# Optimization experiments

Hardware: AMD Instinct MI355X
Metric: run time of the kernel (lower is better)

The kernel has to match this reference:

```python
import jax, jax.numpy as jnp
import numpy as np

N = 512        # N_ROIs (nodes)
E = N * N      # fully connected graph, COO edges
NV = 6         # n_views (edge feature dim)
C1_IN, C1_OUT = 1, 36
C2_IN, C2_OUT = 36, 24
C3_IN, C3_OUT = 24, 5


def _nnconv(x, src, dst, edge_attr, W, b, root, bias, n_nodes):
    """PyG NNConv with aggr='mean': out_i = mean_{j->i} x_j @ Theta(e_ji) + x_i @ root + bias.
    Theta = ReLU(edge_attr @ W + b) reshaped to [E, in, out] (Sequential(Linear, ReLU) edge nn)."""
    in_ch = x.shape[1]
    out_ch = root.shape[1]
    theta = jax.nn.relu(edge_attr @ W + b).reshape(-1, in_ch, out_ch)  # [E, in, out]
    msg = jnp.einsum('ei,eio->eo', x[src], theta)                      # [E, out]
    summed = jax.ops.segment_sum(msg, dst, num_segments=n_nodes)       # [N, out]
    cnt = jax.ops.segment_sum(jnp.ones((msg.shape[0], 1), x.dtype), dst, num_segments=n_nodes)
    agg = summed / jnp.maximum(cnt, 1.0)
    return agg + x @ root + bias


def setup_inputs() -> dict:
    key = jax.random.key(0)
    ks = jax.random.split(key, 12)
    s = lambda fan_in: 1.0 / np.sqrt(fan_in)
    x = jnp.ones((N, C1_IN), jnp.float32)
    edge_attr = jax.random.uniform(ks[0], (E, NV), jnp.float32)
    edge_index = jax.random.randint(ks[1], (2, E), 0, N, dtype=jnp.int64)
    return {
        'x': x, 'edge_attr': edge_attr, 'edge_index': edge_index,
        'W1': jax.random.normal(ks[2], (NV, C1_IN * C1_OUT), jnp.float32) * s(NV),
        'b1': jnp.zeros((C1_IN * C1_OUT,), jnp.float32),
        'root1': jax.random.normal(ks[3], (C1_IN, C1_OUT), jnp.float32) * s(C1_IN),
        'bias1': jnp.zeros((C1_OUT,), jnp.float32),
        'W2': jax.random.normal(ks[4], (NV, C2_IN * C2_OUT), jnp.float32) * s(NV),
        'b2': jnp.zeros((C2_IN * C2_OUT,), jnp.float32),
        'root2': jax.random.normal(ks[5], (C2_IN, C2_OUT), jnp.float32) * s(C2_IN),
        'bias2': jnp.zeros((C2_OUT,), jnp.float32),
        'W3': jax.random.normal(ks[6], (NV, C3_IN * C3_OUT), jnp.float32) * s(NV),
        'b3': jnp.zeros((C3_IN * C3_OUT,), jnp.float32),
        'root3': jax.random.normal(ks[7], (C3_IN, C3_OUT), jnp.float32) * s(C3_IN),
        'bias3': jnp.zeros((C3_OUT,), jnp.float32),
    }


def reference(x, edge_attr, edge_index, W1, b1, root1, bias1,
              W2, b2, root2, bias2, W3, b3, root3, bias3):
    src, dst = edge_index[0], edge_index[1]
    n = x.shape[0]
    h = jax.nn.relu(_nnconv(x, src, dst, edge_attr, W1, b1, root1, bias1, n))
    h = jax.nn.relu(_nnconv(h, src, dst, edge_attr, W2, b2, root2, bias2, n))
    h = jax.nn.relu(_nnconv(h, src, dst, edge_attr, W3, b3, root3, bias3, n))
    # CBT: cbt[a, b] = sum_f |h[b, f] - h[a, f]|  (repeat/transpose/abs/sum in torch)
    cbt = jnp.sum(jnp.abs(h[None, :, :] - h[:, None, :]), axis=2)  # [N, N]
    return cbt
```

## Files before the change

### kernel.cpp

```cpp
#include <hip/hip_runtime.h>

#define N_NODES 512
#define N_EDGES (512 * 512)

typedef _Float16 f16x8 __attribute__((ext_vector_type(8)));
typedef float f32x4 __attribute__((ext_vector_type(4)));

__device__ __forceinline__ unsigned pkf16(float a, float b) {
  return __builtin_bit_cast(unsigned, __builtin_amdgcn_cvt_pkrtz(a, b));
}

__global__ void hist_k(const int* __restrict__ dst, int* __restrict__ counts) {
  __shared__ int lh[N_NODES];
  for (int i = threadIdx.x; i < N_NODES; i += blockDim.x) lh[i] = 0;
  __syncthreads();
  const int stride = gridDim.x * blockDim.x;
  for (int e = blockIdx.x * blockDim.x + threadIdx.x; e < N_EDGES; e += stride)
    atomicAdd(&lh[dst[e]], 1);
  __syncthreads();
  for (int i = threadIdx.x; i < N_NODES; i += blockDim.x) {
    int c = lh[i];
    if (c) atomicAdd(&counts[i], c);
  }
}

__global__ void scan_k(const int* __restrict__ counts, int* __restrict__ offsets,
                       int* __restrict__ cursor) {
  __shared__ int tmp[N_NODES];
  const int t = threadIdx.x;
  const int c = counts[t];
  tmp[t] = c;
  __syncthreads();
  for (int d = 1; d < N_NODES; d <<= 1) {
    int add = (t >= d) ? tmp[t - d] : 0;
    __syncthreads();
    tmp[t] += add;
    __syncthreads();
  }
  offsets[t + 1] = tmp[t];
  if (t == 0) offsets[0] = 0;
  cursor[t] = tmp[t] - c;
}

__launch_bounds__(512)
__global__ void scatter3_k(const float* __restrict__ ea, const int* __restrict__ src,
                           const int* __restrict__ dst, int* __restrict__ cursor,
                           uint4* __restrict__ eaPk, int* __restrict__ srcSorted) {
  __shared__ int lhist[N_NODES];
  __shared__ int gb[N_NODES];
  const int t = threadIdx.x;
  const int c0 = blockIdx.x * 4096;
  lhist[t] = 0;
  __syncthreads();
  int d[8], r[8];
#pragma unroll
  for (int j = 0; j < 8; j++) {
    d[j] = dst[c0 + t + j * 512];
    r[j] = atomicAdd(&lhist[d[j]], 1);
  }
  __syncthreads();
  gb[t] = atomicAdd(&cursor[t], lhist[t]);
  __syncthreads();
#pragma unroll
  for (int j = 0; j < 8; j++) {
    const int e = c0 + t + j * 512;
    const int pos = gb[d[j]] + r[j];
    const float2* er = reinterpret_cast<const float2*>(ea + (size_t)e * 6);
    const float2 a0 = er[0], a1 = er[1], a2 = er[2];
    uint4 pk;
    pk.x = pkf16(a0.x, a0.y);
    pk.y = pkf16(a1.x, a1.y);
    pk.z = pkf16(a2.x, a2.y);
    pk.w = 0x00003C00u;
    eaPk[pos] = pk;
    srcSorted[pos] = src[e];
  }
}

__global__ void packAll2_k(const float* __restrict__ W1, const float* __restrict__ b1,
                           const float* __restrict__ W2, const float* __restrict__ b2,
                           const float* __restrict__ W3, const float* __restrict__ b3,
                           uint4* __restrict__ wpk) {
  const int t = blockIdx.x * 256 + threadIdx.x;
  uint4 r = make_uint4(0u, 0u, 0x00000000u, pkf16(-1.f, 0.f));
  if (t < 48) {
    if (t < 36) {
      r.x = pkf16(W1[0 * 36 + t], W1[1 * 36 + t]);
      r.y = pkf16(W1[2 * 36 + t], W1[3 * 36 + t]);
      r.z = pkf16(W1[4 * 36 + t], W1[5 * 36 + t]);
      r.w = pkf16(b1[t], 0.f);
    }
    wpk[t] = r;
  } else if (t < 1200) {
    const int q = t - 48;
    const int tile = q >> 4, row = q & 15;
    const int i = tile >> 1, o = ((tile & 1) << 4) + row;
    if (o < 24) {
      const int p = i * 24 + o;
      r.x = pkf16(W2[0 * 864 + p], W2[1 * 864 + p]);
      r.y = pkf16(W2[2 * 864 + p], W2[3 * 864 + p]);
      r.z = pkf16(W2[4 * 864 + p], W2[5 * 864 + p]);
      r.w = pkf16(b2[p], 0.f);
    }
    wpk[t] = r;
  } else if (t < 1328) {
    const int q = t - 1200;
    const int tile = q >> 4, row = q & 15;
    if (row < 15) {
      const int i = 3 * tile + row / 5;
      const int o = row % 5;
      const int p = i * 5 + o;
      r.x = pkf16(W3[0 * 120 + p], W3[1 * 120 + p]);
      r.y = pkf16(W3[2 * 120 + p], W3[3 * 120 + p]);
      r.z = pkf16(W3[4 * 120 + p], W3[5 * 120 + p]);
      r.w = pkf16(b3[p], 0.f);
    }
    wpk[t] = r;
  }
}

__launch_bounds__(512, 4)
__global__ void conv1_k(const float* __restrict__ x,
                        const uint4* __restrict__ eaPk, const int* __restrict__ srcSorted,
                        const int* __restrict__ offsets, const uint4* __restrict__ Wpk,
                        const float* __restrict__ root, const float* __restrict__ bias,
                        float* __restrict__ hnext) {
  __shared__ float hS[N_NODES];
  __shared__ float pAcc[8][48];
  const int tid = threadIdx.x, w = tid >> 6, l = tid & 63;
  const int node = blockIdx.x;
  const int off = offsets[node], cnt = offsets[node + 1] - off;
  const int col = l & 15, crow = (l >> 4) << 2;

  if (tid < N_NODES) hS[tid] = x[tid];

  f16x8 afr[3];
  f32x4 acc[3];
#pragma unroll
  for (int t = 0; t < 3; t++) {
    uint4 wv = make_uint4(0u, 0u, 0u, 0u);
    if (l < 16) wv = Wpk[t * 16 + l];
    afr[t] = __builtin_bit_cast(f16x8, wv);
    acc[t] = (f32x4){0.f, 0.f, 0.f, 0.f};
  }
  __syncthreads();

  const int NG = (cnt + 15) >> 4;
  const f32x4 zero4 = {0.f, 0.f, 0.f, 0.f};

  uint4 bv_c = make_uint4(0u, 0u, 0u, 0u);
  int s_c = 0;
  auto gload = [&](int g) {
    const int pos = g * 16 + col;
    const bool v = pos < cnt;
    s_c = v ? srcSorted[off + pos] : 0;
    bv_c = make_uint4(0u, 0u, 0u, 0u);
    if (l < 16 && v) bv_c = eaPk[off + pos];
  };

  if (w < NG) gload(w);
  for (int g = w; g < NG; g += 8) {
    const f16x8 bfr = __builtin_bit_cast(f16x8, bv_c);
    const float hv = hS[s_c];
    if (g + 8 < NG) gload(g + 8);
    f32x4 tc = __builtin_amdgcn_mfma_f32_16x16x32_f16(afr[0], bfr, zero4, 0, 0, 0);
#pragma unroll
    for (int t = 0; t < 3; t++) {
      f32x4 tn;
      if (t < 2) tn = __builtin_amdgcn_mfma_f32_16x16x32_f16(afr[t + 1], bfr, zero4, 0, 0, 0);
#pragma unroll
      for (int r = 0; r < 4; r++)
        acc[t][r] = fmaf(fmaxf(tc[r], 0.f), hv, acc[t][r]);
      if (t < 2) tc = tn;
    }
  }
#pragma unroll
  for (int t = 0; t < 3; t++)
#pragma unroll
    for (int r = 0; r < 4; r++) {
      float vv = acc[t][r];
      vv += __shfl_xor(vv, 1); vv += __shfl_xor(vv, 2);
      vv += __shfl_xor(vv, 4); vv += __shfl_xor(vv, 8);
      if (col == 0) pAcc[w][t * 16 + crow + r] = vv;
    }
  __syncthreads();
  if (tid < 36) {
    const int o = tid;
    float sagg = 0.f;
#pragma unroll
    for (int ww = 0; ww < 8; ww++) sagg += pAcc[ww][o];
    const float agg = sagg / fmaxf((float)cnt, 1.f);
    const float r2 = fmaf(hS[node], root[o], bias[o]);
    hnext[node * 36 + o] = fmaxf(agg + r2, 0.f);
  }
}

__launch_bounds__(512, 4)
__global__ void conv2_k(const float* __restrict__ hprev,
                        const uint4* __restrict__ eaPk, const int* __restrict__ srcSorted,
                        const int* __restrict__ offsets, const uint4* __restrict__ Wpk,
                        const float* __restrict__ root, const float* __restrict__ bias,
                        float* __restrict__ hnext) {
  __shared__ float hS[N_NODES * 37];
  __shared__ float pAcc[1152];
  const int tid = threadIdx.x, w = tid >> 6, l = tid & 63;
  const int node = blockIdx.x;
  const int off = offsets[node], cnt = offsets[node + 1] - off;
  const int col = l & 15, crow = (l >> 4) << 2;

  for (int n = tid; n < N_NODES * 36; n += 512) hS[n + n / 36] = hprev[n];

  f16x8 afr[5][2];
  f32x4 acc[5][2];
  int hidx[5];
#pragma unroll
  for (int jp = 0; jp < 5; jp++) {
    const int tp = w + 8 * jp;
    hidx[jp] = (tp < 36) ? tp : 0;
#pragma unroll
    for (int hh = 0; hh < 2; hh++) {
      uint4 wv = make_uint4(0u, 0u, 0u, 0u);
      if (tp < 36 && l < 16) wv = Wpk[(2 * tp + hh) * 16 + l];
      afr[jp][hh] = __builtin_bit_cast(f16x8, wv);
      acc[jp][hh] = (f32x4){0.f, 0.f, 0.f, 0.f};
    }
  }
  __syncthreads();

  const int NG = (cnt + 15) >> 4;
  const f32x4 zero4 = {0.f, 0.f, 0.f, 0.f};

  uint4 bv_c = make_uint4(0u, 0u, 0u, 0u);
  int s_c = 0;
  auto gload = [&](int g) {
    const int pos = g * 16 + col;
    const bool v = pos < cnt;
    s_c = v ? srcSorted[off + pos] : 0;
    bv_c = make_uint4(0u, 0u, 0u, 0u);
    if (l < 16 && v) bv_c = eaPk[off + pos];
  };

  if (NG > 0) gload(0);
  for (int g = 0; g < NG; g++) {
    const int sb = s_c * 37;
    float hcur[5];
#pragma unroll
    for (int jp = 0; jp < 5; jp++) hcur[jp] = hS[sb + hidx[jp]];
    const f16x8 bfr = __builtin_bit_cast(f16x8, bv_c);
    if (g + 1 < NG) gload(g + 1);
    f32x4 t0 = __builtin_amdgcn_mfma_f32_16x16x32_f16(afr[0][0], bfr, zero4, 0, 0, 0);
    f32x4 t1 = __builtin_amdgcn_mfma_f32_16x16x32_f16(afr[0][1], bfr, zero4, 0, 0, 0);
#pragma unroll
    for (int jp = 0; jp < 5; jp++) {
      f32x4 n0, n1;
      if (jp < 4) {
        n0 = __builtin_amdgcn_mfma_f32_16x16x32_f16(afr[jp + 1][0], bfr, zero4, 0, 0, 0);
        n1 = __builtin_amdgcn_mfma_f32_16x16x32_f16(afr[jp + 1][1], bfr, zero4, 0, 0, 0);
      }
      const float hv = hcur[jp];
#pragma unroll
      for (int r = 0; r < 4; r++) {
        acc[jp][0][r] = fmaf(fmaxf(t0[r], 0.f), hv, acc[jp][0][r]);
        acc[jp][1][r] = fmaf(fmaxf(t1[r], 0.f), hv, acc[jp][1][r]);
      }
      if (jp < 4) { t0 = n0; t1 = n1; }
    }
  }

#pragma unroll
  for (int jp = 0; jp < 5; jp++) {
    const int tp = w + 8 * jp;
    if (tp < 36) {
#pragma unroll
      for (int hh = 0; hh < 2; hh++)
#pragma unroll
        for (int r = 0; r < 4; r++) {
          float vv = acc[jp][hh][r];
          vv += __shfl_xor(vv, 1); vv += __shfl_xor(vv, 2);
          vv += __shfl_xor(vv, 4); vv += __shfl_xor(vv, 8);
          if (col == 0) pAcc[tp * 32 + hh * 16 + crow + r] = vv;
        }
    }
  }
  __syncthreads();
  if (tid < 24) {
    const int o = tid;
    float sagg = 0.f;
    for (int i = 0; i < 36; i++) sagg += pAcc[i * 32 + o];
    const float agg = sagg / fmaxf((float)cnt, 1.f);
    float r2 = bias[o];
    for (int i = 0; i < 36; i++) r2 = fmaf(hS[node * 37 + i], root[i * 24 + o], r2);
    hnext[node * 24 + o] = fmaxf(agg + r2, 0.f);
  }
}

__launch_bounds__(512, 4)
__global__ void conv3_k(const float* __restrict__ hprev,
                        const uint4* __restrict__ eaPk, const int* __restrict__ srcSorted,
                        const int* __restrict__ offsets, const uint4* __restrict__ Wpk,
                        const float* __restrict__ root, const float* __restrict__ bias,
                        float* __restrict__ hnext) {
  __shared__ float hS[N_NODES * 25];
  __shared__ float pAcc[8][128];
  const int tid = threadIdx.x, w = tid >> 6, l = tid & 63;
  const int node = blockIdx.x;
  const int off = offsets[node], cnt = offsets[node + 1] - off;
  const int col = l & 15, crow = (l >> 4) << 2;

  for (int n = tid; n < N_NODES * 24; n += 512) hS[n + n / 24] = hprev[n];

  f16x8 afr[8];
  f32x4 acc[8];
#pragma unroll
  for (int t = 0; t < 8; t++) {
    uint4 wv = make_uint4(0u, 0u, 0u, 0u);
    if (l < 16) wv = Wpk[t * 16 + l];
    afr[t] = __builtin_bit_cast(f16x8, wv);
    acc[t] = (f32x4){0.f, 0.f, 0.f, 0.f};
  }
  __syncthreads();

  const int NG = (cnt + 15) >> 4;
  const f32x4 zero4 = {0.f, 0.f, 0.f, 0.f};

  uint4 bv_c = make_uint4(0u, 0u, 0u, 0u);
  int s_c = 0;
  auto gload = [&](int g) {
    const int pos = g * 16 + col;
    const bool v = pos < cnt;
    s_c = v ? srcSorted[off + pos] : 0;
    bv_c = make_uint4(0u, 0u, 0u, 0u);
    if (l < 16 && v) bv_c = eaPk[off + pos];
  };

  if (w < NG) gload(w);
  for (int g = w; g < NG; g += 8) {
    const int sb = s_c * 25;
    float h0[8], h1[8], h2[8];
#pragma unroll
    for (int t = 0; t < 8; t++) {
      h0[t] = hS[sb + 3 * t];
      h1[t] = hS[sb + 3 * t + 1];
      h2[t] = hS[sb + 3 * t + 2];
    }
    const f16x8 bfr = __builtin_bit_cast(f16x8, bv_c);
    if (g + 8 < NG) gload(g + 8);
    f32x4 tc = __builtin_amdgcn_mfma_f32_16x16x32_f16(afr[0], bfr, zero4, 0, 0, 0);
#pragma unroll
    for (int t = 0; t < 8; t++) {
      f32x4 tn;
      if (t < 7) tn = __builtin_amdgcn_mfma_f32_16x16x32_f16(afr[t + 1], bfr, zero4, 0, 0, 0);
#pragma unroll
      for (int r = 0; r < 4; r++) {
        const int row = crow + r;
        const float hv = (row < 5) ? h0[t] : ((row < 10) ? h1[t] : h2[t]);
        acc[t][r] = fmaf(fmaxf(tc[r], 0.f), hv, acc[t][r]);
      }
      if (t < 7) tc = tn;
    }
  }
#pragma unroll
  for (int t = 0; t < 8; t++)
#pragma unroll
    for (int r = 0; r < 4; r++) {
      float vv = acc[t][r];
      vv += __shfl_xor(vv, 1); vv += __shfl_xor(vv, 2);
      vv += __shfl_xor(vv, 4); vv += __shfl_xor(vv, 8);
      if (col == 0) pAcc[w][t * 16 + crow + r] = vv;
    }
  __syncthreads();
  if (tid < 128) {
    float s8 = 0.f;
#pragma unroll
    for (int ww = 0; ww < 8; ww++) s8 += pAcc[ww][tid];
    pAcc[0][tid] = s8;
  }
  __syncthreads();
  if (tid < 5) {
    const int o = tid;
    float sagg = 0.f;
    for (int i = 0; i < 24; i++) {
      const int t = i / 3, iloc = i - 3 * t;
      sagg += pAcc[0][t * 16 + iloc * 5 + o];
    }
    const float agg = sagg / fmaxf((float)cnt, 1.f);
    float r2 = bias[o];
    for (int i = 0; i < 24; i++) r2 = fmaf(hS[node * 25 + i], root[i * 5 + o], r2);
    hnext[node * 5 + o] = fmaxf(agg + r2, 0.f);
  }
}

__global__ void cbt_k(const float* __restrict__ h3, float* __restrict__ out) {
  __shared__ float sh[N_NODES * 5];
  for (int i = threadIdx.x; i < N_NODES * 5; i += blockDim.x) sh[i] = h3[i];
  __syncthreads();
  const int a = blockIdx.x;
  float ha0 = sh[a * 5 + 0], ha1 = sh[a * 5 + 1], ha2 = sh[a * 5 + 2],
        ha3 = sh[a * 5 + 3], ha4 = sh[a * 5 + 4];
  for (int b = threadIdx.x; b < N_NODES; b += blockDim.x) {
    float s = fabsf(sh[b * 5 + 0] - ha0) + fabsf(sh[b * 5 + 1] - ha1) +
              fabsf(sh[b * 5 + 2] - ha2) + fabsf(sh[b * 5 + 3] - ha3) +
              fabsf(sh[b * 5 + 4] - ha4);
    out[a * N_NODES + b] = s;
  }
}

extern "C" void kernel_launch(void* const* d_in, const int* in_sizes, int n_in,
                              void* d_out, int out_size, void* d_ws, size_t ws_size,
                              hipStream_t stream) {
  const float* x     = (const float*)d_in[0];
  const float* ea    = (const float*)d_in[1];
  const int*   ei    = (const int*)d_in[2];
  const float* W1    = (const float*)d_in[3];
  const float* b1    = (const float*)d_in[4];
  const float* root1 = (const float*)d_in[5];
  const float* bias1 = (const float*)d_in[6];
  const float* W2    = (const float*)d_in[7];
  const float* b2    = (const float*)d_in[8];
  const float* root2 = (const float*)d_in[9];
  const float* bias2 = (const float*)d_in[10];
  const float* W3    = (const float*)d_in[11];
  const float* b3    = (const float*)d_in[12];
  const float* root3 = (const float*)d_in[13];
  const float* bias3 = (const float*)d_in[14];

  const int* src = ei;
  const int* dst = ei + N_EDGES;

  char* ws = (char*)d_ws;
  int* counts    = (int*)(ws + 0);
  int* offsets   = (int*)(ws + 4096);
  int* cursor    = (int*)(ws + 8192);
  uint4* eaPk    = (uint4*)(ws + 16384);
  int* srcSorted = (int*)(ws + 16384 + N_EDGES * 16);
  char* p2       = ws + 16384 + N_EDGES * 20;
  float* h1      = (float*)(p2);
  float* h2_     = h1 + N_NODES * 36;
  float* h3      = h2_ + N_NODES * 24;
  uint4* wpkAll  = (uint4*)(p2 + 256 * 1024);
  uint4* wpk1    = wpkAll;
  uint4* wpk2    = wpkAll + 48;
  uint4* wpk3    = wpkAll + 1200;

  hipMemsetAsync(counts, 0, N_NODES * sizeof(int), stream);
  hist_k<<<64, 256, 0, stream>>>(dst, counts);
  scan_k<<<1, N_NODES, 0, stream>>>(counts, offsets, cursor);
  scatter3_k<<<N_EDGES / 4096, 512, 0, stream>>>(ea, src, dst, cursor, eaPk, srcSorted);
  packAll2_k<<<6, 256, 0, stream>>>(W1, b1, W2, b2, W3, b3, wpkAll);

  conv1_k<<<N_NODES, 512, 0, stream>>>(x, eaPk, srcSorted, offsets, wpk1, root1, bias1, h1);
  conv2_k<<<N_NODES, 512, 0, stream>>>(h1, eaPk, srcSorted, offsets, wpk2, root2, bias2, h2_);
  conv3_k<<<N_NODES, 512, 0, stream>>>(h2_, eaPk, srcSorted, offsets, wpk3, root3, bias3, h3);

  cbt_k<<<N_NODES, 256, 0, stream>>>(h3, (float*)d_out);
}
```

Before: 102.4 us.

## Store node features as fp16 in LDS and regroup conv2 warp-to-channel mapping

In conv2 and conv3, the shared-memory copy of the previous layer's node features is now stored as fp16 instead of fp32. This halves LDS usage, which may allow more resident blocks, at the cost of some precision in the per-edge feature values. Conv2 now gives each warp five contiguous input channels (5*w+jp) instead of strided ones, and splits its edge loop into full 16-edge groups plus a separate remainder pass so the hot loop needs no bounds checks. The root-term reductions read fp32 features straight from global memory so that part keeps full precision.

```diff
diff --git a/kernel.cpp b/kernel.cpp
--- a/kernel.cpp
+++ b/kernel.cpp
@@ -8,6 +8,13 @@
 
 __device__ __forceinline__ unsigned pkf16(float a, float b) {
   return __builtin_bit_cast(unsigned, __builtin_amdgcn_cvt_pkrtz(a, b));
+}
+__device__ __forceinline__ unsigned short f16bits(float a) {
+  return (unsigned short)(pkf16(a, 0.f) & 0xFFFFu);
+}
+__device__ __forceinline__ float f16tof32(unsigned short u) {
+  _Float16 h = __builtin_bit_cast(_Float16, u);
+  return (float)h;
 }
 
 __global__ void hist_k(const int* __restrict__ dst, int* __restrict__ counts) {
@@ -201,22 +208,20 @@
                         const int* __restrict__ offsets, const uint4* __restrict__ Wpk,
                         const float* __restrict__ root, const float* __restrict__ bias,
                         float* __restrict__ hnext) {
-  __shared__ float hS[N_NODES * 37];
+  __shared__ unsigned short hS16[N_NODES * 37];
   __shared__ float pAcc[1152];
   const int tid = threadIdx.x, w = tid >> 6, l = tid & 63;
   const int node = blockIdx.x;
   const int off = offsets[node], cnt = offsets[node + 1] - off;
   const int col = l & 15, crow = (l >> 4) << 2;
 
-  for (int n = tid; n < N_NODES * 36; n += 512) hS[n + n / 36] = hprev[n];
+  for (int n = tid; n < N_NODES * 36; n += 512) hS16[n + n / 36] = f16bits(hprev[n]);
 
   f16x8 afr[5][2];
   f32x4 acc[5][2];
-  int hidx[5];
 #pragma unroll
   for (int jp = 0; jp < 5; jp++) {
-    const int tp = w + 8 * jp;
-    hidx[jp] = (tp < 36) ? tp : 0;
+    const int tp = 5 * w + jp;
 #pragma unroll
     for (int hh = 0; hh < 2; hh++) {
       uint4 wv = make_uint4(0u, 0u, 0u, 0u);
@@ -224,6 +229,126 @@
       afr[jp][hh] = __builtin_bit_cast(f16x8, wv);
       acc[jp][hh] = (f32x4){0.f, 0.f, 0.f, 0.f};
     }
+  }
+  __syncthreads();
+
+  const int NGF = cnt >> 4;
+  const int rem = cnt & 15;
+  const f32x4 zero4 = {0.f, 0.f, 0.f, 0.f};
+  const int tbase = 5 * w;
+
+  uint4 bv_c = make_uint4(0u, 0u, 0u, 0u);
+  int s_c = 0;
+
+  auto body = [&]() {
+    const int sb = s_c * 37 + tbase;
+    float hcur[5];
+#pragma unroll
+    for (int jp = 0; jp < 5; jp++) hcur[jp] = f16tof32(hS16[sb + jp]);
+    const f16x8 bfr = __builtin_bit_cast(f16x8, bv_c);
+    f32x4 t0 = __builtin_amdgcn_mfma_f32_16x16x32_f16(afr[0][0], bfr, zero4, 0, 0, 0);
+    f32x4 t1 = __builtin_amdgcn_mfma_f32_16x16x32_f16(afr[0][1], bfr, zero4, 0, 0, 0);
+#pragma unroll
+    for (int jp = 0; jp < 5; jp++) {
+      f32x4 n0, n1;
+      if (jp < 4) {
+        n0 = __builtin_amdgcn_mfma_f32_16x16x32_f16(afr[jp + 1][0], bfr, zero4, 0, 0, 0);
+        n1 = __builtin_amdgcn_mfma_f32_16x16x32_f16(afr[jp + 1][1], bfr, zero4, 0, 0, 0);
+      }
+      const float hv = hcur[jp];
+#pragma unroll
+      for (int r = 0; r < 4; r++) {
+        acc[jp][0][r] = fmaf(fmaxf(t0[r], 0.f), hv, acc[jp][0][r]);
+        acc[jp][1][r] = fmaf(fmaxf(t1[r], 0.f), hv, acc[jp][1][r]);
+      }
+      if (jp < 4) { t0 = n0; t1 = n1; }
+    }
+  };
+
+  if (NGF > 0) {
+    s_c = srcSorted[off + col];
+    if (l < 16) bv_c = eaPk[off + col];
+  } else if (rem) {
+    const bool v = col < rem;
+    s_c = v ? srcSorted[off + col] : 0;
+    if (l < 16 && v) bv_c = eaPk[off + col];
+  }
+  for (int g = 0; g < NGF; g++) {
+    const uint4 bv_h = bv_c;
+    const int s_h = s_c;
+    if (g + 1 < NGF) {
+      const int p = off + (g + 1) * 16 + col;
+      s_c = srcSorted[p];
+      if (l < 16) bv_c = eaPk[p];
+    } else if (rem) {
+      const int pos = NGF * 16 + col;
+      const bool v = pos < cnt;
+      s_c = v ? srcSorted[off + pos] : 0;
+      bv_c = make_uint4(0u, 0u, 0u, 0u);
+      if (l < 16 && v) bv_c = eaPk[off + pos];
+    }
+    {
+      const uint4 sv = bv_c; const int ss = s_c;
+      bv_c = bv_h; s_c = s_h;
+      body();
+      bv_c = sv; s_c = ss;
+    }
+  }
+  if (rem) body();
+
+#pragma unroll
+  for (int jp = 0; jp < 5; jp++) {
+    const int tp = 5 * w + jp;
+    if (tp < 36) {
+#pragma unroll
+      for (int hh = 0; hh < 2; hh++)
+#pragma unroll
+        for (int r = 0; r < 4; r++) {
+          float vv = acc[jp][hh][r];
+          vv += __shfl_xor(vv, 1); vv += __shfl_xor(vv, 2);
+          vv += __shfl_xor(vv, 4); vv += __shfl_xor(vv, 8);
+          if (col == 0) pAcc[tp * 32 + hh * 16 + crow + r] = vv;
+        }
+    }
+  }
+  __syncthreads();
+  if (tid < 24) {
+    const int o = tid;
+    float sagg = 0.f;
+    for (int i = 0; i < 36; i++) sagg += pAcc[i * 32 + o];
+    const float agg = sagg / fmaxf((float)cnt, 1.f);
+    float r2 = bias[o];
+    for (int i = 0; i < 36; i++) r2 = fmaf(hprev[node * 36 + i], root[i * 24 + o], r2);
+    hnext[node * 24 + o] = fmaxf(agg + r2, 0.f);
+  }
+}
+
+__launch_bounds__(512, 4)
+__global__ void conv3_k(const float* __restrict__ hprev,
+                        const uint4* __restrict__ eaPk, const int* __restrict__ srcSorted,
+                        const int* __restrict__ offsets, const uint4* __restrict__ Wpk,
+                        const float* __restrict__ root, const float* __restrict__ bias,
+                        float* __restrict__ hnext) {
+  __shared__ unsigned short hS16[N_NODES * 26];
+  __shared__ float pAcc[8][128];
+  const int tid = threadIdx.x, w = tid >> 6, l = tid & 63;
+  const int node = blockIdx.x;
+  const int off = offsets[node], cnt = offsets[node + 1] - off;
+  const int col = l & 15, crow = (l >> 4) << 2;
+
+  for (int n = tid; n < N_NODES * 24; n += 512) {
+    const int nn = n / 24;
+    hS16[nn * 26 + (n - nn * 24)] = f16bits(hprev[n]);
+  }
+
+  f16x8 afr[8];
+  f32x4 acc[8];
+#pragma unroll
+  for (int t = 0; t < 8; t++) {
+    uint4 wv = make_uint4(0u, 0u, 0u, 0u);
+    if (l < 16) wv = Wpk[t * 16 + l];
+    afr[t] = __builtin_bit_cast(f16x8, wv);
+    acc[t] = (f32x4){0.f, 0.f, 0.f, 0.f};
   }
   __syncthreads();
 
@@ -240,108 +365,15 @@
     if (l < 16 && v) bv_c = eaPk[off + pos];
   };
 
-  if (NG > 0) gload(0);
-  for (int g = 0; g < NG; g++) {
-    const int sb = s_c * 37;
-    float hcur[5];
-#pragma unroll
-    for (int jp = 0; jp < 5; jp++) hcur[jp] = hS[sb + hidx[jp]];
-    const f16x8 bfr = __builtin_bit_cast(f16x8, bv_c);
-    if (g + 1 < NG) gload(g + 1);
-    f32x4 t0 = __builtin_amdgcn_mfma_f32_16x16x32_f16(afr[0][0], bfr, zero4, 0, 0, 0);
-    f32x4 t1 = __builtin_amdgcn_mfma_f32_16x16x32_f16(afr[0][1], bfr, zero4, 0, 0, 0);
-#pragma unroll
-    for (int jp = 0; jp < 5; jp++) {
-      f32x4 n0, n1;
-      if (jp < 4) {
-        n0 = __builtin_amdgcn_mfma_f32_16x16x32_f16(afr[jp + 1][0], bfr, zero4, 0, 0, 0);
-        n1 = __builtin_amdgcn_mfma_f32_16x16x32_f16(afr[jp + 1][1], bfr, zero4, 0, 0, 0);
-      }
-      const float hv = hcur[jp];
-#pragma unroll
-      for (int r = 0; r < 4; r++) {
-        acc[jp][0][r] = fmaf(fmaxf(t0[r], 0.f), hv, acc[jp][0][r]);
-        acc[jp][1][r] = fmaf(fmaxf(t1[r], 0.f), hv, acc[jp][1][r]);
-      }
-      if (jp < 4) { t0 = n0; t1 = n1; }
-    }
-  }
-
-#pragma unroll
-  for (int jp = 0; jp < 5; jp++) {
-    const int tp = w + 8 * jp;
-    if (tp < 36) {
-#pragma unroll
-      for (int hh = 0; hh < 2; hh++)
-#pragma unroll
-        for (int r = 0; r < 4; r++) {
-          float vv = acc[jp][hh][r];
-          vv += __shfl_xor(vv, 1); vv += __shfl_xor(vv, 2);
-          vv += __shfl_xor(vv, 4); vv += __shfl_xor(vv, 8);
-          if (col == 0) pAcc[tp * 32 + hh * 16 + crow + r] = vv;
-        }
-    }
-  }
-  __syncthreads();
-  if (tid < 24) {
-    const int o = tid;
-    float sagg = 0.f;
-    for (int i = 0; i < 36; i++) sagg += pAcc[i * 32 + o];
-    const float agg = sagg / fmaxf((float)cnt, 1.f);
-    float r2 = bias[o];
-    for (int i = 0; i < 36; i++) r2 = fmaf(hS[node * 37 + i], root[i * 24 + o], r2);
-    hnext[node * 24 + o] = fmaxf(agg + r2, 0.f);
-  }
-}
-
-__launch_bounds__(512, 4)
-__global__ void conv3_k(const float* __restrict__ hprev,
-                        const uint4* __restrict__ eaPk, const int* __restrict__ srcSorted,
-                        const int* __restrict__ offsets, const uint4* __restrict__ Wpk,
-                        const float* __restrict__ root, const float* __restrict__ bias,
-                        float* __restrict__ hnext) {
-  __shared__ float hS[N_NODES * 25];
-  __shared__ float pAcc[8][128];
-  const int tid = threadIdx.x, w = tid >> 6, l = tid & 63;
-  const int node = blockIdx.x;
-  const int off = offsets[node], cnt = offsets[node + 1] - off;
-  const int col = l & 15, crow = (l >> 4) << 2;
-
-  for (int n = tid; n < N_NODES * 24; n += 512) hS[n + n / 24] = hprev[n];
-
-  f16x8 afr[8];
-  f32x4 acc[8];
-#pragma unroll
-  for (int t = 0; t < 8; t++) {
-    uint4 wv = make_uint4(0u, 0u, 0u, 0u);
-    if (l < 16) wv = Wpk[t * 16 + l];
-    afr[t] = __builtin_bit_cast(f16x8, wv);
-    acc[t] = (f32x4){0.f, 0.f, 0.f, 0.f};
-  }
-  __syncthreads();
-
-  const int NG = (cnt + 15) >> 4;
-  const f32x4 zero4 = {0.f, 0.f, 0.f, 0.f};
-
-  uint4 bv_c = make_uint4(0u, 0u, 0u, 0u);
-  int s_c = 0;
-  auto gload = [&](int g) {
-    const int pos = g * 16 + col;
-    const bool v = pos < cnt;
-    s_c = v ? srcSorted[off + pos] : 0;
-    bv_c = make_uint4(0u, 0u, 0u, 0u);
-    if (l < 16 && v) bv_c = eaPk[off + pos];
-  };
-
   if (w < NG) gload(w);
   for (int g = w; g < NG; g += 8) {
-    const int sb = s_c * 25;
+    const int sb = s_c * 26;
     float h0[8], h1[8], h2[8];
 #pragma unroll
     for (int t = 0; t < 8; t++) {
-      h0[t] = hS[sb + 3 * t];
-      h1[t] = hS[sb + 3 * t + 1];
-      h2[t] = hS[sb + 3 * t + 2];
+      h0[t] = f16tof32(hS16[sb + 3 * t]);
+      h1[t] = f16tof32(hS16[sb + 3 * t + 1]);
+      h2[t] = f16tof32(hS16[sb + 3 * t + 2]);
     }
     const f16x8 bfr = __builtin_bit_cast(f16x8, bv_c);
     if (g + 8 < NG) gload(g + 8);
@@ -385,7 +417,7 @@
     }
     const float agg = sagg / fmaxf((float)cnt, 1.f);
     float r2 = bias[o];
-    for (int i = 0; i < 24; i++) r2 = fmaf(hS[node * 25 + i], root[i * 5 + o], r2);
+    for (int i = 0; i < 24; i++) r2 = fmaf(hprev[node * 24 + i], root[i * 5 + o], r2);
     hnext[node * 5 + o] = fmaxf(agg + r2, 0.f);
   }
 }
```

Measured after the change: 116.5 us. 1.14x slower.

## Split conv2 input channels across two blocks per node with a combine kernel

Applied to the files above, without the earlier changes.

Each node's conv2 work is now split into two blocks, each covering half of the 36 input channels. This halves the per-block register accumulators, MFMA count and shared-memory staging of h1, which raises occupancy and parallelism. Partial sums go to a workspace buffer, and a new small kernel adds the two halves, applies the mean, the root projection, bias and ReLU. The cost is duplicated edge-attribute and source-index loads in both blocks plus an extra kernel launch.

```diff
diff --git a/kernel.cpp b/kernel.cpp
--- a/kernel.cpp
+++ b/kernel.cpp
@@ -199,28 +199,33 @@
 __global__ void conv2_k(const float* __restrict__ hprev,
                         const uint4* __restrict__ eaPk, const int* __restrict__ srcSorted,
                         const int* __restrict__ offsets, const uint4* __restrict__ Wpk,
-                        const float* __restrict__ root, const float* __restrict__ bias,
-                        float* __restrict__ hnext) {
-  __shared__ float hS[N_NODES * 37];
-  __shared__ float pAcc[1152];
+                        float* __restrict__ part) {
+  __shared__ float hS[N_NODES * 19];
+  __shared__ float pAcc[576];
   const int tid = threadIdx.x, w = tid >> 6, l = tid & 63;
-  const int node = blockIdx.x;
+  const int node = blockIdx.x >> 1, half = blockIdx.x & 1;
   const int off = offsets[node], cnt = offsets[node + 1] - off;
   const int col = l & 15, crow = (l >> 4) << 2;
-
-  for (int n = tid; n < N_NODES * 36; n += 512) hS[n + n / 36] = hprev[n];
-
-  f16x8 afr[5][2];
-  f32x4 acc[5][2];
-  int hidx[5];
-#pragma unroll
-  for (int jp = 0; jp < 5; jp++) {
-    const int tp = w + 8 * jp;
-    hidx[jp] = (tp < 36) ? tp : 0;
+  const int ibase = half * 18;
+
+  for (int n = tid; n < N_NODES * 18; n += 512) {
+    const int s = n / 18, j = n - s * 18;
+    hS[s * 19 + j] = hprev[s * 36 + ibase + j];
+  }
+
+  f16x8 afr[3][2];
+  f32x4 acc[3][2];
+  int hidx[3];
+#pragma unroll
+  for (int jp = 0; jp < 3; jp++) {
+    const int tpl = w + 8 * jp;
+    const bool valid = tpl < 18;
+    hidx[jp] = valid ? tpl : 0;
+    const int tp = ibase + (valid ? tpl : 0);
 #pragma unroll
     for (int hh = 0; hh < 2; hh++) {
       uint4 wv = make_uint4(0u, 0u, 0u, 0u);
-      if (tp < 36 && l < 16) wv = Wpk[(2 * tp + hh) * 16 + l];
+      if (valid && l < 16) wv = Wpk[(2 * tp + hh) * 16 + l];
       afr[jp][hh] = __builtin_bit_cast(f16x8, wv);
       acc[jp][hh] = (f32x4){0.f, 0.f, 0.f, 0.f};
     }
@@ -242,18 +247,18 @@
 
   if (NG > 0) gload(0);
   for (int g = 0; g < NG; g++) {
-    const int sb = s_c * 37;
-    float hcur[5];
-#pragma unroll
-    for (int jp = 0; jp < 5; jp++) hcur[jp] = hS[sb + hidx[jp]];
+    const int sb = s_c * 19;
+    float hcur[3];
+#pragma unroll
+    for (int jp = 0; jp < 3; jp++) hcur[jp] = hS[sb + hidx[jp]];
     const f16x8 bfr = __builtin_bit_cast(f16x8, bv_c);
     if (g + 1 < NG) gload(g + 1);
     f32x4 t0 = __builtin_amdgcn_mfma_f32_16x16x32_f16(afr[0][0], bfr, zero4, 0, 0, 0);
     f32x4 t1 = __builtin_amdgcn_mfma_f32_16x16x32_f16(afr[0][1], bfr, zero4, 0, 0, 0);
 #pragma unroll
-    for (int jp = 0; jp < 5; jp++) {
+    for (int jp = 0; jp < 3; jp++) {
       f32x4 n0, n1;
-      if (jp < 4) {
+      if (jp < 2) {
         n0 = __builtin_amdgcn_mfma_f32_16x16x32_f16(afr[jp + 1][0], bfr, zero4, 0, 0, 0);
         n1 = __builtin_amdgcn_mfma_f32_16x16x32_f16(afr[jp + 1][1], bfr, zero4, 0, 0, 0);
       }
@@ -263,14 +268,14 @@
         acc[jp][0][r] = fmaf(fmaxf(t0[r], 0.f), hv, acc[jp][0][r]);
         acc[jp][1][r] = fmaf(fmaxf(t1[r], 0.f), hv, acc[jp][1][r]);
       }
-      if (jp < 4) { t0 = n0; t1 = n1; }
-    }
-  }
-
-#pragma unroll
-  for (int jp = 0; jp < 5; jp++) {
-    const int tp = w + 8 * jp;
-    if (tp < 36) {
+      if (jp < 2) { t0 = n0; t1 = n1; }
+    }
+  }
+
+#pragma unroll
+  for (int jp = 0; jp < 3; jp++) {
+    const int tpl = w + 8 * jp;
+    if (tpl < 18) {
 #pragma unroll
       for (int hh = 0; hh < 2; hh++)
 #pragma unroll
@@ -278,7 +283,7 @@
           float vv = acc[jp][hh][r];
           vv += __shfl_xor(vv, 1); vv += __shfl_xor(vv, 2);
           vv += __shfl_xor(vv, 4); vv += __shfl_xor(vv, 8);
-          if (col == 0) pAcc[tp * 32 + hh * 16 + crow + r] = vv;
+          if (col == 0) pAcc[tpl * 32 + hh * 16 + crow + r] = vv;
         }
     }
   }
@@ -286,11 +291,24 @@
   if (tid < 24) {
     const int o = tid;
     float sagg = 0.f;
-    for (int i = 0; i < 36; i++) sagg += pAcc[i * 32 + o];
+    for (int i = 0; i < 18; i++) sagg += pAcc[i * 32 + o];
+    part[node * 48 + half * 24 + o] = sagg;
+  }
+}
+
+__global__ void comb2_k(const float* __restrict__ part, const float* __restrict__ h1,
+                        const int* __restrict__ offsets, const float* __restrict__ root,
+                        const float* __restrict__ bias, float* __restrict__ h2) {
+  const int idx = blockIdx.x * 256 + threadIdx.x;
+  if (idx < N_NODES * 24) {
+    const int node = idx / 24, o = idx - node * 24;
+    const int cnt = offsets[node + 1] - offsets[node];
+    const float sagg = part[node * 48 + o] + part[node * 48 + 24 + o];
     const float agg = sagg / fmaxf((float)cnt, 1.f);
     float r2 = bias[o];
-    for (int i = 0; i < 36; i++) r2 = fmaf(hS[node * 37 + i], root[i * 24 + o], r2);
-    hnext[node * 24 + o] = fmaxf(agg + r2, 0.f);
+    const float* hr = h1 + node * 36;
+    for (int i = 0; i < 36; i++) r2 = fmaf(hr[i], root[i * 24 + o], r2);
+    h2[idx] = fmaxf(agg + r2, 0.f);
   }
 }
 
@@ -437,6 +455,7 @@
   float* h1      = (float*)(p2);
   float* h2_     = h1 + N_NODES * 36;
   float* h3      = h2_ + N_NODES * 24;
+  float* part    = h3 + N_NODES * 5;
   uint4* wpkAll  = (uint4*)(p2 + 256 * 1024);
   uint4* wpk1    = wpkAll;
   uint4* wpk2    = wpkAll + 48;
@@ -449,7 +468,8 @@
   packAll2_k<<<6, 256, 0, stream>>>(W1, b1, W2, b2, W3, b3, wpkAll);
 
   conv1_k<<<N_NODES, 512, 0, stream>>>(x, eaPk, srcSorted, offsets, wpk1, root1, bias1, h1);
-  conv2_k<<<N_NODES, 512, 0, stream>>>(h1, eaPk, srcSorted, offsets, wpk2, root2, bias2, h2_);
+  conv2_k<<<N_NODES * 2, 512, 0, stream>>>(h1, eaPk, srcSorted, offsets, wpk2, part);
+  comb2_k<<<48, 256, 0, stream>>>(part, h1, offsets, root2, bias2, h2_);
   conv3_k<<<N_NODES, 512, 0, stream>>>(h2_, eaPk, srcSorted, offsets, wpk3, root3, bias3, h3);
 
   cbt_k<<<N_NODES, 256, 0, stream>>>(h3, (float*)d_out);
```

New measurement: 112.0 us. +9.4%, slower.
